# Kernel optimization log

Measured on AMD Instinct MI355X. Metric: run time of the kernel, lower is better.

The kernel has to match this reference:

```python
import jax, jax.numpy as jnp
import numpy as np

N, E, D_IN, H, L, C = 50000, 800000, 500, 256, 4, 7
ALPHA, GAMMA, EPS = 0.5, 0.5, 0.1  # self-loop weight, parallel-edge weight, FAConv eps
LN_EPS = 1e-5


def setup_inputs() -> dict:
    key = jax.random.key(0)
    ks = jax.random.split(key, 8)
    x = jax.random.normal(ks[0], (N, D_IN), jnp.float32)
    src = jax.random.randint(ks[1], (E,), 0, N, jnp.int32)
    dst = jax.random.randint(ks[2], (E,), 0, N, jnp.int32)
    dst = jnp.where(dst == src, (dst + 1) % N, dst)  # ensure no self-loops (remove_self_loops is then a no-op)
    edge_index = jnp.stack([src, dst])
    s_in = 1.0 / np.sqrt(D_IN)
    s_h = 1.0 / np.sqrt(H)
    W_init = jax.random.uniform(ks[3], (H, D_IN), jnp.float32, -s_in, s_in)
    b_init = jnp.zeros((H,), jnp.float32)
    att_l = jax.random.uniform(ks[4], (L, H), jnp.float32, -s_h, s_h)
    att_r = jax.random.uniform(ks[5], (L, H), jnp.float32, -s_h, s_h)
    ln_g = jnp.ones((L, H), jnp.float32)
    ln_b = jnp.zeros((L, H), jnp.float32)
    W_last = jax.random.uniform(ks[6], (C, H), jnp.float32, -s_h, s_h)
    b_last = jnp.zeros((C,), jnp.float32)
    return dict(x=x, edge_index=edge_index, W_init=W_init, b_init=b_init,
                att_l=att_l, att_r=att_r, ln_g=ln_g, ln_b=ln_b,
                W_last=W_last, b_last=b_last)


def _layernorm(x, g, b):
    mu = jnp.mean(x, axis=-1, keepdims=True)
    var = jnp.var(x, axis=-1, keepdims=True)
    return (x - mu) * jax.lax.rsqrt(var + LN_EPS) * g + b


def reference(x, edge_index, W_init, b_init, att_l, att_r, ln_g, ln_b, W_last, b_last):
    num_nodes = x.shape[0]
    num_edges = edge_index.shape[1]
    x = x @ W_init.T + b_init  # [N, H]
    x0 = x
    # add self-loops after parallel edges
    loop = jnp.arange(num_nodes, dtype=edge_index.dtype)
    src = jnp.concatenate([edge_index[0], loop])
    dst = jnp.concatenate([edge_index[1], loop])
    ew = jnp.concatenate([jnp.full((num_edges,), GAMMA, x.dtype),
                          jnp.full((num_nodes,), ALPHA, x.dtype)])
    for i in range(L):
        # FAConv: alpha_e = tanh(att_l.x_src + att_r.x_dst); msg = x_src * alpha_e * ew
        al = x @ att_l[i]  # [N]
        ar = x @ att_r[i]  # [N]
        a_e = jnp.tanh(al[src] + ar[dst]) * ew  # [E+N]
        msg = x[src] * a_e[:, None]            # [E+N, H]
        agg = jax.ops.segment_sum(msg, dst, num_segments=num_nodes)
        x = agg + EPS * x0
        if i != L - 1:
            x = _layernorm(jax.nn.relu(x), ln_g[i], ln_b[i])
            # F.dropout with p=0.0 is identity
    emb = x @ W_last.T + b_last  # [N, C]
    return emb, jax.nn.log_softmax(emb, axis=1)
```

## Files before the change

### kernel.cpp

```cpp
#include <hip/hip_runtime.h>
#include <hip/hip_fp16.h>

#define N_NODES 50000
#define N_EDGES 800000
#define D_IN_K  500
#define K_PAD   512
#define H_DIM   256
#define N_CLS   7
#define ALPHA_W 0.5f
#define GAMMA_W 0.5f
#define EPS_W   0.1f
#define LN_EPS_W 1e-5f

#define SCAN_B 256
#define SCAN_NB ((N_NODES + SCAN_B - 1) / SCAN_B)

typedef unsigned short u16;
typedef unsigned int   u32;
typedef _Float16 f16;
typedef __attribute__((ext_vector_type(8))) _Float16 f16x8;
typedef __attribute__((ext_vector_type(4))) float    f32x4;
typedef __attribute__((ext_vector_type(8))) unsigned short u16x8;

__device__ __forceinline__ float h2f(u16 v) {
    __half h;
    *reinterpret_cast<u16*>(&h) = v;
    return __half2float(h);
}
__device__ __forceinline__ u16 f2h(float f) {
    __half h = __float2half_rn(f);
    return *reinterpret_cast<u16*>(&h);
}
__device__ __forceinline__ int clampN(int v) {
    return (v < 0) ? 0 : ((v >= N_NODES) ? N_NODES - 1 : v);
}

__global__ __launch_bounds__(256) void sentinel_kernel(float* out, int n) {
    int i = blockIdx.x * blockDim.x + threadIdx.x;
    if (i < n) out[i] = 2.0f;
}

__global__ __launch_bounds__(256) void zero_kernel(int* p, int n) {
    int i = blockIdx.x * blockDim.x + threadIdx.x;
    if (i < n) p[i] = 0;
}

__global__ __launch_bounds__(256) void hist_kernel(const int* __restrict__ dst, int* __restrict__ deg, int e) {
    int i = blockIdx.x * blockDim.x + threadIdx.x;
    if (i < e) atomicAdd(&deg[clampN(dst[i])], 1);
}

__global__ __launch_bounds__(SCAN_B) void scan_a(const int* __restrict__ deg, int* __restrict__ row_ptr,
                                                 int* __restrict__ bsum) {
    __shared__ int sdata[SCAN_B];
    int t = threadIdx.x;
    int i = blockIdx.x * SCAN_B + t;
    int v = (i < N_NODES) ? deg[i] : 0;
    sdata[t] = v;
    __syncthreads();
#pragma unroll
    for (int off = 1; off < SCAN_B; off <<= 1) {
        int a = (t >= off) ? sdata[t - off] : 0;
        __syncthreads();
        sdata[t] += a;
        __syncthreads();
    }
    if (i < N_NODES) row_ptr[i] = sdata[t] - v;
    if (t == SCAN_B - 1) bsum[blockIdx.x] = sdata[t];
}

__global__ __launch_bounds__(SCAN_B) void scan_b(int* __restrict__ bsum, int* __restrict__ boff,
                                                 int* __restrict__ row_ptr) {
    __shared__ int sdata[SCAN_B];
    int t = threadIdx.x;
    int v = (t < SCAN_NB) ? bsum[t] : 0;
    sdata[t] = v;
    __syncthreads();
#pragma unroll
    for (int off = 1; off < SCAN_B; off <<= 1) {
        int a = (t >= off) ? sdata[t - off] : 0;
        __syncthreads();
        sdata[t] += a;
        __syncthreads();
    }
    if (t < SCAN_NB) boff[t] = sdata[t] - v;
    if (t == SCAN_B - 1) row_ptr[N_NODES] = sdata[t];
}

__global__ __launch_bounds__(SCAN_B) void scan_c(int* __restrict__ row_ptr, const int* __restrict__ boff) {
    int i = blockIdx.x * SCAN_B + threadIdx.x;
    if (i < N_NODES) row_ptr[i] += boff[blockIdx.x];
}

__global__ __launch_bounds__(256) void scatter_kernel(const int* __restrict__ src, const int* __restrict__ dst,
                                                      const int* __restrict__ row_ptr, int* __restrict__ deg,
                                                      int* __restrict__ srcS, int e) {
    int i = blockIdx.x * blockDim.x + threadIdx.x;
    if (i < e) {
        int d = clampN(dst[i]);
        int old = atomicSub(&deg[d], 1);
        int pos = row_ptr[d] + old - 1;
        if (pos >= 0 && pos < e) srcS[pos] = clampN(src[i]);
    }
}

__global__ __launch_bounds__(256) void convert_w(const float* __restrict__ W, f16* __restrict__ W16) {
    int i = blockIdx.x * 256 + threadIdx.x;
    int n = i >> 9, k = i & (K_PAD - 1);
    W16[i] = (k < D_IN_K) ? (f16)W[n * D_IN_K + k] : (f16)0.f;
}

#define GW_STRIDE 520
#define GA_BUF    (16 * GW_STRIDE)

__device__ __forceinline__ f16x8 stage_load(const float* __restrict__ X, int tile, int r, int sc) {
    const float* p = X + (long)(tile * 16 + r) * D_IN_K + sc;
    f16x8 v;
    if (sc + 8 <= D_IN_K) {
        float4 lo = *(const float4*)(p);
        float4 hi = *(const float4*)(p + 4);
        v[0] = (f16)lo.x; v[1] = (f16)lo.y; v[2] = (f16)lo.z; v[3] = (f16)lo.w;
        v[4] = (f16)hi.x; v[5] = (f16)hi.y; v[6] = (f16)hi.z; v[7] = (f16)hi.w;
    } else {
#pragma unroll
        for (int t = 0; t < 8; t++)
            v[t] = (sc + t < D_IN_K) ? (f16)p[t] : (f16)0.f;
    }
    return v;
}

__global__ __launch_bounds__(1024) void mfma_gemm5(const float* __restrict__ X,
                                                   const f16* __restrict__ W16,
                                                   const float* __restrict__ bias,
                                                   u16* __restrict__ out) {
    __shared__ __align__(16) f16 alds[2 * GA_BUF];

    int tid  = threadIdx.x;
    int w    = tid >> 6;
    int lane = tid & 63;
    int m    = lane & 15;
    int quad = lane >> 4;
    int h    = w * 16 + m;

    f16x8 bfrag[16];
    {
        const f16* wb = W16 + (long)h * K_PAD + quad * 8;
#pragma unroll
        for (int kc = 0; kc < 16; kc++)
            bfrag[kc] = *(const f16x8*)(wb + kc * 32);
    }
    float bv = bias[h];

    int sr = w;
    int sc = lane * 8;

    int nt = N_NODES / 16;
    int t  = blockIdx.x;
    int buf = 0;

    if (t < nt) {
        f16x8 sv = stage_load(X, t, sr, sc);
        *(f16x8*)&alds[sr * GW_STRIDE + sc] = sv;
    }
    __syncthreads();

    while (t < nt) {
        int tn = t + (int)gridDim.x;
        bool hn = (tn < nt);
        f16x8 nsv;
        if (hn) nsv = stage_load(X, tn, sr, sc);

        f32x4 acc = (f32x4){0.f, 0.f, 0.f, 0.f};
        const f16* ab = &alds[buf * GA_BUF + m * GW_STRIDE + quad * 8];
#pragma unroll
        for (int kc = 0; kc < 16; kc++) {
            f16x8 a = *(const f16x8*)(ab + kc * 32);
            acc = __builtin_amdgcn_mfma_f32_16x16x32_f16(a, bfrag[kc], acc, 0, 0, 0);
        }

        long nb = (long)t * 16 + quad * 4;
#pragma unroll
        for (int r = 0; r < 4; r++)
            out[(nb + r) * H_DIM + h] = f2h(acc[r] + bv);

        if (hn) *(f16x8*)&alds[(buf ^ 1) * GA_BUF + sr * GW_STRIDE + sc] = nsv;
        __syncthreads();
        buf ^= 1;
        t = tn;
    }
}

__global__ __launch_bounds__(256) void alar_kernel(const u16* __restrict__ x,
                                                   const float* __restrict__ attl,
                                                   const float* __restrict__ attr,
                                                   float* __restrict__ al, float* __restrict__ ar, int n) {
    int w = (blockIdx.x * blockDim.x + threadIdx.x) >> 6;
    int lane = threadIdx.x & 63;
    if (w >= n) return;
    int col = lane * 4;
    ushort4 xv = *(const ushort4*)(x + (long)w * H_DIM + col);
    float4 lv = *(const float4*)(attl + col);
    float4 rv = *(const float4*)(attr + col);
    float x0 = h2f(xv.x), x1 = h2f(xv.y), x2 = h2f(xv.z), x3 = h2f(xv.w);
    float pl = x0 * lv.x + x1 * lv.y + x2 * lv.z + x3 * lv.w;
    float pr = x0 * rv.x + x1 * rv.y + x2 * rv.z + x3 * rv.w;
#pragma unroll
    for (int off = 32; off >= 1; off >>= 1) {
        pl += __shfl_xor(pl, off);
        pr += __shfl_xor(pr, off);
    }
    if (lane == 0) { al[w] = pl; ar[w] = pr; }
}

__global__ __launch_bounds__(256) void layer_kernel3(const u16* __restrict__ xin,
                                                     const u16* __restrict__ x0,
                                                     const float* __restrict__ alIn,
                                                     float* __restrict__ alOut,
                                                     float* __restrict__ ar,
                                                     const int* __restrict__ row_ptr,
                                                     const int* __restrict__ srcS,
                                                     const float* __restrict__ g,
                                                     const float* __restrict__ b,
                                                     const float* __restrict__ attlN,
                                                     const float* __restrict__ attrN,
                                                     u16* __restrict__ xout,
                                                     const float* __restrict__ Wl,
                                                     const float* __restrict__ bl,
                                                     float* __restrict__ outF,
                                                     int n, int mode) {
    int w = (blockIdx.x * blockDim.x + threadIdx.x) >> 6;
    int lane = threadIdx.x & 63;
    if (w >= n) return;
    int half = lane >> 5;
    int sub  = lane & 31;
    int col  = sub * 8;

    float arn = ar[w];
    float aself = ALPHA_W * tanhf(alIn[w] + arn);

    float acc[8];
    if (half == 0) {
        u16x8 xs  = *(const u16x8*)(xin + (long)w * H_DIM + col);
        u16x8 x0v = *(const u16x8*)(x0  + (long)w * H_DIM + col);
#pragma unroll
        for (int k = 0; k < 8; k++) acc[k] = aself * h2f(xs[k]) + EPS_W * h2f(x0v[k]);
    } else {
#pragma unroll
        for (int k = 0; k < 8; k++) acc[k] = 0.f;
    }

    int e0 = row_ptr[w], e1 = row_ptr[w + 1];
    for (int base = e0; base < e1; base += 64) {
        int cnt = e1 - base; if (cnt > 64) cnt = 64;
        int s = 0; float a = 0.f;
        if (lane < cnt) {
            s = clampN(srcS[base + lane]);
            a = GAMMA_W * tanhf(alIn[s] + arn);
        }
        for (int j = 0; j < cnt; j += 8) {
            int i0 = j + half, i1 = j + 2 + half, i2 = j + 4 + half, i3 = j + 6 + half;
            int s0 = __shfl(s, i0), s1 = __shfl(s, i1), s2 = __shfl(s, i2), s3 = __shfl(s, i3);
            float c0 = __shfl(a, i0), c1 = __shfl(a, i1), c2 = __shfl(a, i2), c3 = __shfl(a, i3);
            u16x8 v0 = *(const u16x8*)(xin + (long)s0 * H_DIM + col);
            u16x8 v1 = *(const u16x8*)(xin + (long)s1 * H_DIM + col);
            u16x8 v2 = *(const u16x8*)(xin + (long)s2 * H_DIM + col);
            u16x8 v3 = *(const u16x8*)(xin + (long)s3 * H_DIM + col);
#pragma unroll
            for (int k = 0; k < 8; k++) {
                acc[k] = fmaf(c0, h2f(v0[k]), acc[k]);
                acc[k] = fmaf(c1, h2f(v1[k]), acc[k]);
                acc[k] = fmaf(c2, h2f(v2[k]), acc[k]);
                acc[k] = fmaf(c3, h2f(v3[k]), acc[k]);
            }
        }
    }

#pragma unroll
    for (int k = 0; k < 8; k++) acc[k] += __shfl(acc[k], lane ^ 32);

    if (mode == 0) {
        float v[8];
        float sum = 0.f, sq = 0.f;
#pragma unroll
        for (int k = 0; k < 8; k++) {
            v[k] = fmaxf(acc[k], 0.f);
            sum += v[k];
            sq  += v[k] * v[k];
        }
#pragma unroll
        for (int off = 16; off >= 1; off >>= 1) {
            sum += __shfl_xor(sum, off);
            sq  += __shfl_xor(sq, off);
        }
        float mu = sum * (1.f / 256.f);
        float var = fmaxf(sq * (1.f / 256.f) - mu * mu, 0.f);
        float rstd = rsqrtf(var + LN_EPS_W);
        float4 ga = *(const float4*)(g + col);
        float4 gb = *(const float4*)(g + col + 4);
        float4 ba = *(const float4*)(b + col);
        float4 bb = *(const float4*)(b + col + 4);
        float gg[8]  = {ga.x, ga.y, ga.z, ga.w, gb.x, gb.y, gb.z, gb.w};
        float bbv[8] = {ba.x, ba.y, ba.z, ba.w, bb.x, bb.y, bb.z, bb.w};
        float4 la = *(const float4*)(attlN + col);
        float4 lb = *(const float4*)(attlN + col + 4);
        float4 ra = *(const float4*)(attrN + col);
        float4 rb = *(const float4*)(attrN + col + 4);
        float ll[8] = {la.x, la.y, la.z, la.w, lb.x, lb.y, lb.z, lb.w};
        float rr[8] = {ra.x, ra.y, ra.z, ra.w, rb.x, rb.y, rb.z, rb.w};
        float pl = 0.f, pr = 0.f;
        u16x8 o;
#pragma unroll
        for (int k = 0; k < 8; k++) {
            float val = (v[k] - mu) * rstd * gg[k] + bbv[k];
            o[k] = f2h(val);
            pl += val * ll[k];
            pr += val * rr[k];
        }
#pragma unroll
        for (int off = 16; off >= 1; off >>= 1) {
            pl += __shfl_xor(pl, off);
            pr += __shfl_xor(pr, off);
        }
        if (lane == 0) { alOut[w] = pl; ar[w] = pr; }
        if (half == 0) *(u16x8*)(xout + (long)w * H_DIM + col) = o;
    } else {
        float p[N_CLS];
#pragma unroll
        for (int c = 0; c < N_CLS; c++) {
            const float* wr = Wl + c * H_DIM + col;
            float4 wa = *(const float4*)(wr);
            float4 wb = *(const float4*)(wr + 4);
            p[c] = acc[0] * wa.x + acc[1] * wa.y + acc[2] * wa.z + acc[3] * wa.w
                 + acc[4] * wb.x + acc[5] * wb.y + acc[6] * wb.z + acc[7] * wb.w;
        }
#pragma unroll
        for (int off = 16; off >= 1; off >>= 1) {
#pragma unroll
            for (int c = 0; c < N_CLS; c++) p[c] += __shfl_xor(p[c], off);
        }
        if (lane == 0) {
            float e[N_CLS];
            float m = -1e30f;
#pragma unroll
            for (int c = 0; c < N_CLS; c++) {
                e[c] = p[c] + bl[c];
                m = fmaxf(m, e[c]);
            }
            float sx = 0.f;
#pragma unroll
            for (int c = 0; c < N_CLS; c++) sx += expf(e[c] - m);
            float lse = logf(sx);
#pragma unroll
            for (int c = 0; c < N_CLS; c++) {
                outF[(long)w * N_CLS + c] = e[c];
                outF[(long)N_NODES * N_CLS + (long)w * N_CLS + c] = e[c] - m - lse;
            }
        }
    }
}

extern "C" void kernel_launch(void* const* d_in, const int* in_sizes, int n_in,
                              void* d_out, int out_size, void* d_ws, size_t ws_size,
                              hipStream_t stream) {
    const float* x_in   = (const float*)d_in[0];
    const int*   ei     = (const int*)d_in[1];
    const float* W_init = (const float*)d_in[2];
    const float* b_init = (const float*)d_in[3];
    const float* att_l  = (const float*)d_in[4];
    const float* att_r  = (const float*)d_in[5];
    const float* ln_g   = (const float*)d_in[6];
    const float* ln_b   = (const float*)d_in[7];
    const float* W_last = (const float*)d_in[8];
    const float* b_last = (const float*)d_in[9];
    float* out = (float*)d_out;

    const size_t OFF_X0  = 0;
    const size_t OFF_XA  = 25600000;
    const size_t OFF_XB  = 51200000;
    const size_t OFF_AL  = 76800000;
    const size_t OFF_AR  = 77000000;
    const size_t OFF_DEG = 77200000;
    const size_t OFF_RP  = 77400000;
    const size_t OFF_SRC = 77600064;
    const size_t OFF_BS  = 80800064;
    const size_t OFF_BO  = 80801088;
    const size_t WS_NEED = 80802112;

    if (ws_size < WS_NEED) {
        sentinel_kernel<<<(out_size + 255) / 256, 256, 0, stream>>>(out, out_size);
        return;
    }

    char* ws = (char*)d_ws;
    u16* x0  = (u16*)(ws + OFF_X0);
    u16* xA  = (u16*)(ws + OFF_XA);
    u16* xB  = (u16*)(ws + OFF_XB);
    f16* W16 = (f16*)(ws + OFF_AL);
    float* al  = (float*)(ws + OFF_AL);
    float* ar  = (float*)(ws + OFF_AR);
    float* al2 = (float*)(ws + OFF_DEG);
    int* deg     = (int*)(ws + OFF_DEG);
    int* row_ptr = (int*)(ws + OFF_RP);
    int* srcS    = (int*)(ws + OFF_SRC);
    int* bsum    = (int*)(ws + OFF_BS);
    int* boff    = (int*)(ws + OFF_BO);

    const int* e_src = ei;
    const int* e_dst = ei + N_EDGES;

    int zb = (N_NODES + 255) / 256;
    zero_kernel<<<zb, 256, 0, stream>>>(deg, N_NODES);
    int eb = (N_EDGES + 255) / 256;
    hist_kernel<<<eb, 256, 0, stream>>>(e_dst, deg, N_EDGES);
    scan_a<<<SCAN_NB, SCAN_B, 0, stream>>>(deg, row_ptr, bsum);
    scan_b<<<1, SCAN_B, 0, stream>>>(bsum, boff, row_ptr);
    scan_c<<<SCAN_NB, SCAN_B, 0, stream>>>(row_ptr, boff);
    scatter_kernel<<<eb, 256, 0, stream>>>(e_src, e_dst, row_ptr, deg, srcS, N_EDGES);

    convert_w<<<(H_DIM * K_PAD) / 256, 256, 0, stream>>>(W_init, W16);
    mfma_gemm5<<<256, 1024, 0, stream>>>(x_in, W16, b_init, x0);

    int nb = (N_NODES * 64 + 255) / 256;
    alar_kernel<<<nb, 256, 0, stream>>>(x0, att_l, att_r, al, ar, N_NODES);

    const u16* bufs_in[4]   = {x0, xA, xB, xA};
    u16* bufs_out[4]        = {xA, xB, xA, xB};
    const float* al_in[4]   = {al, al2, al, al2};
    float* al_out[4]        = {al2, al, al2, al};
    for (int i = 0; i < 4; i++) {
        int nxt = (i < 3) ? (i + 1) : i;
        layer_kernel3<<<nb, 256, 0, stream>>>(bufs_in[i], x0, al_in[i], al_out[i], ar,
                                              row_ptr, srcS,
                                              ln_g + i * H_DIM, ln_b + i * H_DIM,
                                              att_l + nxt * H_DIM, att_r + nxt * H_DIM,
                                              bufs_out[i], W_last, b_last, out,
                                              N_NODES, (i < 3) ? 0 : 1);
    }
}
```

Measured before the change: 548.7 us.

## Software-pipeline neighbor row gathers and use fma_mix in layer kernel

The edge aggregation loop now prefetches the next group of four neighbor rows while accumulating the current group, so gather latency is meant to overlap with arithmetic. The fp16-to-fp32 convert plus FMA is replaced with inline v_fma_mix_f32 asm that consumes half values directly, cutting ALU instructions. The block size is reduced from 256 to 128 threads (two nodes per block). The prefetch raises register pressure, and the first prefetch reads rows for lanes beyond cnt whose shuffled index defaults to 0, which is safe but wasted.

```diff
diff --git a/kernel.cpp b/kernel.cpp
--- a/kernel.cpp
+++ b/kernel.cpp
@@ -33,6 +33,18 @@
 }
 __device__ __forceinline__ int clampN(int v) {
     return (v < 0) ? 0 : ((v >= N_NODES) ? N_NODES - 1 : v);
+}
+
+__device__ __forceinline__ void fma_mix_row(float* acc, u16x8 v, float c) {
+    uint4 p = *reinterpret_cast<const uint4*>(&v);
+    asm("v_fma_mix_f32 %0, %1, %2, %0 op_sel:[0,0,0] op_sel_hi:[1,0,0]" : "+v"(acc[0]) : "v"(p.x), "v"(c));
+    asm("v_fma_mix_f32 %0, %1, %2, %0 op_sel:[1,0,0] op_sel_hi:[1,0,0]" : "+v"(acc[1]) : "v"(p.x), "v"(c));
+    asm("v_fma_mix_f32 %0, %1, %2, %0 op_sel:[0,0,0] op_sel_hi:[1,0,0]" : "+v"(acc[2]) : "v"(p.y), "v"(c));
+    asm("v_fma_mix_f32 %0, %1, %2, %0 op_sel:[1,0,0] op_sel_hi:[1,0,0]" : "+v"(acc[3]) : "v"(p.y), "v"(c));
+    asm("v_fma_mix_f32 %0, %1, %2, %0 op_sel:[0,0,0] op_sel_hi:[1,0,0]" : "+v"(acc[4]) : "v"(p.z), "v"(c));
+    asm("v_fma_mix_f32 %0, %1, %2, %0 op_sel:[1,0,0] op_sel_hi:[1,0,0]" : "+v"(acc[5]) : "v"(p.z), "v"(c));
+    asm("v_fma_mix_f32 %0, %1, %2, %0 op_sel:[0,0,0] op_sel_hi:[1,0,0]" : "+v"(acc[6]) : "v"(p.w), "v"(c));
+    asm("v_fma_mix_f32 %0, %1, %2, %0 op_sel:[1,0,0] op_sel_hi:[1,0,0]" : "+v"(acc[7]) : "v"(p.w), "v"(c));
 }
 
 __global__ __launch_bounds__(256) void sentinel_kernel(float* out, int n) {
@@ -212,7 +224,7 @@
     if (lane == 0) { al[w] = pl; ar[w] = pr; }
 }
 
-__global__ __launch_bounds__(256) void layer_kernel3(const u16* __restrict__ xin,
+__global__ __launch_bounds__(128) void layer_kernel4(const u16* __restrict__ xin,
                                                      const u16* __restrict__ x0,
                                                      const float* __restrict__ alIn,
                                                      float* __restrict__ alOut,
@@ -228,7 +240,7 @@
                                                      const float* __restrict__ bl,
                                                      float* __restrict__ outF,
                                                      int n, int mode) {
-    int w = (blockIdx.x * blockDim.x + threadIdx.x) >> 6;
+    int w = (blockIdx.x * 128 + threadIdx.x) >> 6;
     int lane = threadIdx.x & 63;
     if (w >= n) return;
     int half = lane >> 5;
@@ -257,21 +269,35 @@
             s = clampN(srcS[base + lane]);
             a = GAMMA_W * tanhf(alIn[s] + arn);
         }
+        u16x8 v0, v1, v2, v3;
+        {
+            int s0 = __shfl(s, half),     s1 = __shfl(s, 2 + half);
+            int s2 = __shfl(s, 4 + half), s3 = __shfl(s, 6 + half);
+            v0 = *(const u16x8*)(xin + (long)s0 * H_DIM + col);
+            v1 = *(const u16x8*)(xin + (long)s1 * H_DIM + col);
+            v2 = *(const u16x8*)(xin + (long)s2 * H_DIM + col);
+            v3 = *(const u16x8*)(xin + (long)s3 * H_DIM + col);
+        }
         for (int j = 0; j < cnt; j += 8) {
-            int i0 = j + half, i1 = j + 2 + half, i2 = j + 4 + half, i3 = j + 6 + half;
-            int s0 = __shfl(s, i0), s1 = __shfl(s, i1), s2 = __shfl(s, i2), s3 = __shfl(s, i3);
-            float c0 = __shfl(a, i0), c1 = __shfl(a, i1), c2 = __shfl(a, i2), c3 = __shfl(a, i3);
-            u16x8 v0 = *(const u16x8*)(xin + (long)s0 * H_DIM + col);
-            u16x8 v1 = *(const u16x8*)(xin + (long)s1 * H_DIM + col);
-            u16x8 v2 = *(const u16x8*)(xin + (long)s2 * H_DIM + col);
-            u16x8 v3 = *(const u16x8*)(xin + (long)s3 * H_DIM + col);
-#pragma unroll
-            for (int k = 0; k < 8; k++) {
-                acc[k] = fmaf(c0, h2f(v0[k]), acc[k]);
-                acc[k] = fmaf(c1, h2f(v1[k]), acc[k]);
-                acc[k] = fmaf(c2, h2f(v2[k]), acc[k]);
-                acc[k] = fmaf(c3, h2f(v3[k]), acc[k]);
+            u16x8 n0, n1, n2, n3;
+            bool more = (j + 8 < cnt);
+            if (more) {
+                int t0 = __shfl(s, j + 8 + half),  int_t1; (void)0;
+                int t1 = __shfl(s, j + 10 + half);
+                int t2 = __shfl(s, j + 12 + half);
+                int t3 = __shfl(s, j + 14 + half);
+                n0 = *(const u16x8*)(xin + (long)t0 * H_DIM + col);
+                n1 = *(const u16x8*)(xin + (long)t1 * H_DIM + col);
+                n2 = *(const u16x8*)(xin + (long)t2 * H_DIM + col);
+                n3 = *(const u16x8*)(xin + (long)t3 * H_DIM + col);
             }
+            float c0 = __shfl(a, j + half),     c1 = __shfl(a, j + 2 + half);
+            float c2 = __shfl(a, j + 4 + half), c3 = __shfl(a, j + 6 + half);
+            fma_mix_row(acc, v0, c0);
+            fma_mix_row(acc, v1, c1);
+            fma_mix_row(acc, v2, c2);
+            fma_mix_row(acc, v3, c3);
+            if (more) { v0 = n0; v1 = n1; v2 = n2; v3 = n3; }
         }
     }
 
@@ -423,13 +449,14 @@
     int nb = (N_NODES * 64 + 255) / 256;
     alar_kernel<<<nb, 256, 0, stream>>>(x0, att_l, att_r, al, ar, N_NODES);
 
+    int lb = (N_NODES + 1) / 2;
     const u16* bufs_in[4]   = {x0, xA, xB, xA};
     u16* bufs_out[4]        = {xA, xB, xA, xB};
     const float* al_in[4]   = {al, al2, al, al2};
     float* al_out[4]        = {al2, al, al2, al};
     for (int i = 0; i < 4; i++) {
         int nxt = (i < 3) ? (i + 1) : i;
-        layer_kernel3<<<nb, 256, 0, stream>>>(bufs_in[i], x0, al_in[i], al_out[i], ar,
+        layer_kernel4<<<lb, 128, 0, stream>>>(bufs_in[i], x0, al_in[i], al_out[i], ar,
                                               row_ptr, srcS,
                                               ln_g + i * H_DIM, ln_b + i * H_DIM,
                                               att_l + nxt * H_DIM, att_r + nxt * H_DIM,
```

New measurement: 546.6 us. No clear change (-0.4%).

## Map one node per half-wave in layer kernel and use fp16 fma_mix

Applied to the files above, without the earlier changes.

Each 64-lane wave now handles two nodes, one per 32-lane half, instead of splitting one node's edges across the halves. This drops the final cross-half accumulator shuffle and halves the grid size. The inner accumulate now uses inline v_fma_mix_f32 so fp16 values feed the fp32 FMA directly, without separate conversion instructions. In exchange, the two halves loop to the larger of their two degrees, so degree imbalance leaves some lanes idle.

```diff
diff --git a/kernel.cpp b/kernel.cpp
--- a/kernel.cpp
+++ b/kernel.cpp
@@ -33,6 +33,18 @@
 }
 __device__ __forceinline__ int clampN(int v) {
     return (v < 0) ? 0 : ((v >= N_NODES) ? N_NODES - 1 : v);
+}
+
+__device__ __forceinline__ void fma_mix_row(float* acc, u16x8 v, float c) {
+    uint4 p = *reinterpret_cast<const uint4*>(&v);
+    asm("v_fma_mix_f32 %0, %1, %2, %0 op_sel:[0,0,0] op_sel_hi:[1,0,0]" : "+v"(acc[0]) : "v"(p.x), "v"(c));
+    asm("v_fma_mix_f32 %0, %1, %2, %0 op_sel:[1,0,0] op_sel_hi:[1,0,0]" : "+v"(acc[1]) : "v"(p.x), "v"(c));
+    asm("v_fma_mix_f32 %0, %1, %2, %0 op_sel:[0,0,0] op_sel_hi:[1,0,0]" : "+v"(acc[2]) : "v"(p.y), "v"(c));
+    asm("v_fma_mix_f32 %0, %1, %2, %0 op_sel:[1,0,0] op_sel_hi:[1,0,0]" : "+v"(acc[3]) : "v"(p.y), "v"(c));
+    asm("v_fma_mix_f32 %0, %1, %2, %0 op_sel:[0,0,0] op_sel_hi:[1,0,0]" : "+v"(acc[4]) : "v"(p.z), "v"(c));
+    asm("v_fma_mix_f32 %0, %1, %2, %0 op_sel:[1,0,0] op_sel_hi:[1,0,0]" : "+v"(acc[5]) : "v"(p.z), "v"(c));
+    asm("v_fma_mix_f32 %0, %1, %2, %0 op_sel:[0,0,0] op_sel_hi:[1,0,0]" : "+v"(acc[6]) : "v"(p.w), "v"(c));
+    asm("v_fma_mix_f32 %0, %1, %2, %0 op_sel:[1,0,0] op_sel_hi:[1,0,0]" : "+v"(acc[7]) : "v"(p.w), "v"(c));
 }
 
 __global__ __launch_bounds__(256) void sentinel_kernel(float* out, int n) {
@@ -212,7 +224,7 @@
     if (lane == 0) { al[w] = pl; ar[w] = pr; }
 }
 
-__global__ __launch_bounds__(256) void layer_kernel3(const u16* __restrict__ xin,
+__global__ __launch_bounds__(256) void layer_kernel5(const u16* __restrict__ xin,
                                                      const u16* __restrict__ x0,
                                                      const float* __restrict__ alIn,
                                                      float* __restrict__ alOut,
@@ -228,55 +240,53 @@
                                                      const float* __restrict__ bl,
                                                      float* __restrict__ outF,
                                                      int n, int mode) {
-    int w = (blockIdx.x * blockDim.x + threadIdx.x) >> 6;
+    int pair = (blockIdx.x * 256 + threadIdx.x) >> 6;
     int lane = threadIdx.x & 63;
-    if (w >= n) return;
     int half = lane >> 5;
     int sub  = lane & 31;
-    int col  = sub * 8;
+    int w = pair * 2 + half;
+    if (w >= n) w = n - 1;
+    int col = sub * 8;
 
     float arn = ar[w];
     float aself = ALPHA_W * tanhf(alIn[w] + arn);
 
     float acc[8];
-    if (half == 0) {
+    {
         u16x8 xs  = *(const u16x8*)(xin + (long)w * H_DIM + col);
         u16x8 x0v = *(const u16x8*)(x0  + (long)w * H_DIM + col);
 #pragma unroll
         for (int k = 0; k < 8; k++) acc[k] = aself * h2f(xs[k]) + EPS_W * h2f(x0v[k]);
-    } else {
-#pragma unroll
-        for (int k = 0; k < 8; k++) acc[k] = 0.f;
     }
 
     int e0 = row_ptr[w], e1 = row_ptr[w + 1];
-    for (int base = e0; base < e1; base += 64) {
-        int cnt = e1 - base; if (cnt > 64) cnt = 64;
+    int d  = e1 - e0;
+    int dmax = max(d, __shfl(d, lane ^ 32));
+
+    for (int cb = 0; cb < dmax; cb += 32) {
+        int cnt  = d - cb;
+        int cmax = dmax - cb; if (cmax > 32) cmax = 32;
         int s = 0; float a = 0.f;
-        if (lane < cnt) {
-            s = clampN(srcS[base + lane]);
+        if (sub < cnt) {
+            s = clampN(srcS[e0 + cb + sub]);
             a = GAMMA_W * tanhf(alIn[s] + arn);
         }
-        for (int j = 0; j < cnt; j += 8) {
-            int i0 = j + half, i1 = j + 2 + half, i2 = j + 4 + half, i3 = j + 6 + half;
-            int s0 = __shfl(s, i0), s1 = __shfl(s, i1), s2 = __shfl(s, i2), s3 = __shfl(s, i3);
-            float c0 = __shfl(a, i0), c1 = __shfl(a, i1), c2 = __shfl(a, i2), c3 = __shfl(a, i3);
+        int hb = half << 5;
+        for (int j = 0; j < cmax; j += 4) {
+            int   s0 = __shfl(s, hb + j),     s1 = __shfl(s, hb + j + 1);
+            int   s2 = __shfl(s, hb + j + 2), s3 = __shfl(s, hb + j + 3);
+            float c0 = __shfl(a, hb + j),     c1 = __shfl(a, hb + j + 1);
+            float c2 = __shfl(a, hb + j + 2), c3 = __shfl(a, hb + j + 3);
             u16x8 v0 = *(const u16x8*)(xin + (long)s0 * H_DIM + col);
             u16x8 v1 = *(const u16x8*)(xin + (long)s1 * H_DIM + col);
             u16x8 v2 = *(const u16x8*)(xin + (long)s2 * H_DIM + col);
             u16x8 v3 = *(const u16x8*)(xin + (long)s3 * H_DIM + col);
-#pragma unroll
-            for (int k = 0; k < 8; k++) {
-                acc[k] = fmaf(c0, h2f(v0[k]), acc[k]);
-                acc[k] = fmaf(c1, h2f(v1[k]), acc[k]);
-                acc[k] = fmaf(c2, h2f(v2[k]), acc[k]);
-                acc[k] = fmaf(c3, h2f(v3[k]), acc[k]);
-            }
-        }
-    }
-
-#pragma unroll
-    for (int k = 0; k < 8; k++) acc[k] += __shfl(acc[k], lane ^ 32);
+            fma_mix_row(acc, v0, c0);
+            fma_mix_row(acc, v1, c1);
+            fma_mix_row(acc, v2, c2);
+            fma_mix_row(acc, v3, c3);
+        }
+    }
 
     if (mode == 0) {
         float v[8];
@@ -321,8 +331,8 @@
             pl += __shfl_xor(pl, off);
             pr += __shfl_xor(pr, off);
         }
-        if (lane == 0) { alOut[w] = pl; ar[w] = pr; }
-        if (half == 0) *(u16x8*)(xout + (long)w * H_DIM + col) = o;
+        if (sub == 0) { alOut[w] = pl; ar[w] = pr; }
+        *(u16x8*)(xout + (long)w * H_DIM + col) = o;
     } else {
         float p[N_CLS];
 #pragma unroll
@@ -338,7 +348,7 @@
 #pragma unroll
             for (int c = 0; c < N_CLS; c++) p[c] += __shfl_xor(p[c], off);
         }
-        if (lane == 0) {
+        if (sub == 0) {
             float e[N_CLS];
             float m = -1e30f;
 #pragma unroll
@@ -423,13 +433,14 @@
     int nb = (N_NODES * 64 + 255) / 256;
     alar_kernel<<<nb, 256, 0, stream>>>(x0, att_l, att_r, al, ar, N_NODES);
 
+    int lb = (N_NODES + 7) / 8;
     const u16* bufs_in[4]   = {x0, xA, xB, xA};
     u16* bufs_out[4]        = {xA, xB, xA, xB};
     const float* al_in[4]   = {al, al2, al, al2};
     float* al_out[4]        = {al2, al, al2, al};
     for (int i = 0; i < 4; i++) {
         int nxt = (i < 3) ? (i + 1) : i;
-        layer_kernel3<<<nb, 256, 0, stream>>>(bufs_in[i], x0, al_in[i], al_out[i], ar,
+        layer_kernel5<<<lb, 256, 0, stream>>>(bufs_in[i], x0, al_in[i], al_out[i], ar,
                                               row_ptr, srcS,
                                               ln_g + i * H_DIM, ln_b + i * H_DIM,
                                               att_l + nxt * H_DIM, att_r + nxt * H_DIM,
```

Result: faster. 522.8 us (-4.7%).
